# Kernel optimization log

Measured on AMD Instinct MI355X. Metric: run time of the kernel, lower is better.

The kernel has to match this reference:

```python
import jax, jax.numpy as jnp
import numpy as np

N0, N1, N2 = 100000, 20000, 4000   # nodes per hierarchy level
F, H, C = 128, 128, 10             # num_features, hidden_dim, num_classes
E0, E1, E2 = 1600000, 320000, 64000  # intra-level edges (avg degree 16)
EPS = 1e-5                          # BatchNorm eps


def setup_inputs() -> dict:
    key = jax.random.key(0)
    ks = jax.random.split(key, 16)
    s = 0.05
    return {
        "x": jax.random.normal(ks[0], (N0, F), jnp.float32),
        "ei0": jax.random.randint(ks[1], (2, E0), 0, N0),
        "ei1": jax.random.randint(ks[2], (2, E1), 0, N1),
        "ei2": jax.random.randint(ks[3], (2, E2), 0, N2),
        "parent1": jax.random.randint(ks[4], (N0,), 0, N1),
        "parent2": jax.random.randint(ks[5], (N1,), 0, N2),
        "W0": jax.random.normal(ks[6], (F, H), jnp.float32) * s,
        "b0": jnp.zeros((H,), jnp.float32),
        "W1": jax.random.normal(ks[7], (H, H), jnp.float32) * s,
        "b1": jnp.zeros((H,), jnp.float32),
        "W2": jax.random.normal(ks[8], (H, H), jnp.float32) * s,
        "b2": jnp.zeros((H,), jnp.float32),
        "W3": jax.random.normal(ks[9], (2 * H, H), jnp.float32) * s,
        "b3": jnp.zeros((H,), jnp.float32),
        "W4": jax.random.normal(ks[10], (2 * H, C), jnp.float32) * s,
        "b4": jnp.zeros((C,), jnp.float32),
        "pW": jax.random.normal(ks[11], (4, H, H), jnp.float32) * s,
        "pb": jnp.zeros((4, H), jnp.float32),
        "pgamma": jnp.ones((4, H), jnp.float32),
        "pbeta": jnp.zeros((4, H), jnp.float32),
        "pmean": jax.random.normal(ks[12], (4, H), jnp.float32) * 0.1,
        "pvar": jax.random.uniform(ks[13], (4, H), jnp.float32, 0.5, 1.5),
    }


def _gcn(x, ei, W, b):
    # GCNConv: add self loops, symmetric D^-1/2 (A+I) D^-1/2 normalization.
    n = x.shape[0]
    loops = jnp.arange(n)
    row = jnp.concatenate([ei[0], loops])  # source nodes
    col = jnp.concatenate([ei[1], loops])  # target nodes
    deg = jax.ops.segment_sum(jnp.ones(row.shape, x.dtype), col, num_segments=n)
    dis = deg ** -0.5  # deg >= 1 because of self loops
    norm = dis[row] * dis[col]
    xw = x @ W
    out = jax.ops.segment_sum(norm[:, None] * xw[row], col, num_segments=n)
    return out + b


def _pool_nn(y, W, b, g, beta, mean, var):
    # SEPooling nn: Linear -> ReLU -> BatchNorm1d (eval mode, running stats)
    y = jax.nn.relu(y @ W + b)
    return (y - mean) * (g / jnp.sqrt(var + EPS)) + beta


def reference(x, ei0, ei1, ei2, parent1, parent2,
              W0, b0, W1, b1, W2, b2, W3, b3, W4, b4,
              pW, pb, pgamma, pbeta, pmean, pvar):
    relu = jax.nn.relu
    # down path (dropout is identity in eval mode)
    h0 = relu(_gcn(x, ei0, W0, b0))  # [N0,H]; stored skip xs[0]
    p = jax.ops.segment_sum(h0, parent1, num_segments=N1)  # scatter-add children -> parents
    x1 = relu(_pool_nn(p, pW[0], pb[0], pgamma[0], pbeta[0], pmean[0], pvar[0]))
    h1 = relu(_gcn(x1, ei1, W1, b1))  # [N1,H]; stored skip xs[1]
    p = jax.ops.segment_sum(h1, parent2, num_segments=N2)
    x2 = relu(_pool_nn(p, pW[1], pb[1], pgamma[1], pbeta[1], pmean[1], pvar[1]))
    # up path: conv, unpool (gather parent feature per child), concat skip
    h = relu(_gcn(x2, ei2, W2, b2))  # [N2,H]
    xu = relu(_pool_nn(h[parent2], pW[2], pb[2], pgamma[2], pbeta[2], pmean[2], pvar[2]))  # [N1,H]
    xc = jnp.concatenate([xu, h1], axis=1)  # [N1,2H]
    h = relu(_gcn(xc, ei1, W3, b3))  # [N1,H]
    xu = relu(_pool_nn(h[parent1], pW[3], pb[3], pgamma[3], pbeta[3], pmean[3], pvar[3]))  # [N0,H]
    xc = jnp.concatenate([xu, h0], axis=1)  # [N0,2H]
    out = _gcn(xc, ei0, W4, b4)  # [N0,C]
    return jax.nn.log_softmax(out, axis=-1)
```

## Files before the change

kernel.cpp:

```cpp
#include <hip/hip_runtime.h>
#include <math.h>

#define N0 100000
#define N1 20000
#define N2 4000
#define HDIM 128
#define E0C 1600000
#define E1C 320000
#define E2C 64000
#define EPSBN 1e-5f

typedef unsigned int u32;
typedef float f32x4 __attribute__((ext_vector_type(4)));
typedef short bf16x8 __attribute__((ext_vector_type(8)));

union FragU { uint4 u; bf16x8 h; };
__device__ __forceinline__ bf16x8 asbf(uint4 v) { FragU x; x.u = v; return x.h; }

__device__ __forceinline__ float bl(u32 p) { return __uint_as_float(p << 16); }
__device__ __forceinline__ float bh(u32 p) { return __uint_as_float(p & 0xFFFF0000u); }
__device__ __forceinline__ u32 pack2(float a, float b) {
    u32 ua = __float_as_uint(a), ub = __float_as_uint(b);
    ua = (ua + 0x7FFFu + ((ua >> 16) & 1u)) >> 16;
    ub = (ub + 0x7FFFu + ((ub >> 16) & 1u)) >> 16;
    return ua | (ub << 16);
}

#define OFF0 0
#define OFF1 (N0)
#define OFF2 (N0 + N1)
#define OFF3 (N0 + N1 + N2)
#define OFF4 (N0 + N1 + N2 + N1)
#define OFFT (N0 + N1 + N2 + N1 + N2)

#define S0 (E0C)
#define S1 (E0C + E1C)
#define S2 (E0C + E1C + E2C)
#define S3 (E0C + E1C + E2C + N0)
#define S4 (E0C + E1C + E2C + N0 + N1)

#define NBUCK ((OFFT + 1023) / 1024)
#define ITEMS_PER_BLK 4096
#define NBA ((S4 + ITEMS_PER_BLK - 1) / ITEMS_PER_BLK)
#define BH_N (NBUCK * NBA)
#define NBLK2 ((BH_N + 1023) / 1024)


__device__ __forceinline__ void item_full(int g,
    const int* __restrict__ ei0r, const int* __restrict__ ei0c,
    const int* __restrict__ ei1r, const int* __restrict__ ei1c,
    const int* __restrict__ ei2r, const int* __restrict__ ei2c,
    const int* __restrict__ p1, const int* __restrict__ p2,
    int& concat, int& payload)
{
    if (g < S0)      { concat = ei0c[g];             payload = ei0r[g]; }
    else if (g < S1) { int i = g - S0; concat = OFF1 + ei1c[i]; payload = ei1r[i]; }
    else if (g < S2) { int i = g - S1; concat = OFF2 + ei2c[i]; payload = ei2r[i]; }
    else if (g < S3) { int i = g - S2; concat = OFF3 + p1[i];   payload = i; }
    else             { int i = g - S3; concat = OFF4 + p2[i];   payload = i; }
}

__device__ __forceinline__ int item_concat(int g,
    const int* __restrict__ ei0c, const int* __restrict__ ei1c, const int* __restrict__ ei2c,
    const int* __restrict__ p1, const int* __restrict__ p2)
{
    if (g < S0)      return ei0c[g];
    else if (g < S1) return OFF1 + ei1c[g - S0];
    else if (g < S2) return OFF2 + ei2c[g - S1];
    else if (g < S3) return OFF3 + p1[g - S2];
    else             return OFF4 + p2[g - S3];
}

__global__ __launch_bounds__(256) void binhist_kernel(
    const int* __restrict__ ei0c, const int* __restrict__ ei1c, const int* __restrict__ ei2c,
    const int* __restrict__ p1, const int* __restrict__ p2,
    int* __restrict__ blockHist)
{
    __shared__ int hist[NBUCK];
    int tid = threadIdx.x, blk = blockIdx.x;
    for (int i = tid; i < NBUCK; i += 256) hist[i] = 0;
    __syncthreads();
    int base = blk * ITEMS_PER_BLK;
    #pragma unroll
    for (int k = 0; k < 16; k++) {
        int g = base + k * 256 + tid;
        if (g < S4) {
            int c = item_concat(g, ei0c, ei1c, ei2c, p1, p2);
            atomicAdd(&hist[c >> 10], 1);
        }
    }
    __syncthreads();
    for (int b = tid; b < NBUCK; b += 256) blockHist[b * NBA + blk] = hist[b];
}

__global__ __launch_bounds__(256) void scan_k1(const int* __restrict__ c, int* __restrict__ bsum, int n) {
    int t = threadIdx.x;
    int base = blockIdx.x * 1024 + t * 4;
    int s = 0;
    #pragma unroll
    for (int j = 0; j < 4; j++) {
        int idx = base + j;
        if (idx < n) s += c[idx];
    }
    #pragma unroll
    for (int o = 32; o > 0; o >>= 1) s += __shfl_down(s, o, 64);
    __shared__ int ws[4];
    if ((t & 63) == 0) ws[t >> 6] = s;
    __syncthreads();
    if (t == 0) bsum[blockIdx.x] = ws[0] + ws[1] + ws[2] + ws[3];
}

__global__ __launch_bounds__(256) void scan_k2(int* __restrict__ bsum, int* __restrict__ totalOut, int nb) {
    int t = threadIdx.x;
    int v = (t < nb) ? bsum[t] : 0;
    __shared__ int ts[256];
    ts[t] = v;
    __syncthreads();
    for (int o = 1; o < 256; o <<= 1) {
        int u = (t >= o) ? ts[t - o] : 0;
        __syncthreads();
        ts[t] += u;
        __syncthreads();
    }
    if (t < nb) bsum[t] = ts[t] - v;
    if (t == nb - 1) *totalOut = ts[t];
}

__global__ __launch_bounds__(256) void scan_k3(const int* __restrict__ c, const int* __restrict__ bsum,
                                               const int* __restrict__ total,
                                               int* __restrict__ S, int n) {
    int t = threadIdx.x;
    int base = blockIdx.x * 1024 + t * 4;
    int v[4];
    #pragma unroll
    for (int j = 0; j < 4; j++) v[j] = (base + j < n) ? c[base + j] : 0;
    int tsum = v[0] + v[1] + v[2] + v[3];
    __shared__ int ts[256];
    ts[t] = tsum;
    __syncthreads();
    for (int o = 1; o < 256; o <<= 1) {
        int u = (t >= o) ? ts[t - o] : 0;
        __syncthreads();
        ts[t] += u;
        __syncthreads();
    }
    int run = bsum[blockIdx.x] + ts[t] - tsum;
    #pragma unroll
    for (int j = 0; j < 4; j++) {
        if (base + j < n) { S[base + j] = run; run += v[j]; }
    }
    if (blockIdx.x == 0 && t == 0) S[n] = *total;
}

__global__ __launch_bounds__(256) void binfill_kernel(
    const int* __restrict__ ei0r, const int* __restrict__ ei0c,
    const int* __restrict__ ei1r, const int* __restrict__ ei1c,
    const int* __restrict__ ei2r, const int* __restrict__ ei2c,
    const int* __restrict__ p1, const int* __restrict__ p2,
    const int* __restrict__ OfsAbs, u32* __restrict__ binPair)
{
    __shared__ int cur[NBUCK];
    int tid = threadIdx.x, blk = blockIdx.x;
    for (int i = tid; i < NBUCK; i += 256) cur[i] = OfsAbs[i * NBA + blk];
    __syncthreads();
    int base = blk * ITEMS_PER_BLK;
    #pragma unroll
    for (int k = 0; k < 16; k++) {
        int g = base + k * 256 + tid;
        if (g < S4) {
            int c, p;
            item_full(g, ei0r, ei0c, ei1r, ei1c, ei2r, ei2c, p1, p2, c, p);
            int pos = atomicAdd(&cur[c >> 10], 1);
            binPair[pos] = ((u32)(c & 1023) << 17) | (u32)p;
        }
    }
}

__global__ __launch_bounds__(256) void bucket_build_kernel(
    const u32* __restrict__ binPair, const int* __restrict__ OfsAbs,
    int* __restrict__ rpAll, int* __restrict__ srcU,
    float* __restrict__ dis0, float* __restrict__ dis1, float* __restrict__ dis2)
{
    __shared__ int cnt_l[1024];
    __shared__ int rp_l[1024];
    __shared__ int ts[256];
    int b = blockIdx.x, tid = threadIdx.x;
    int start = OfsAbs[b * NBA];
    int end = (b + 1 < NBUCK) ? OfsAbs[(b + 1) * NBA] : S4;
    int d0 = b << 10;
    int nd = OFFT - d0; if (nd > 1024) nd = 1024;

    for (int i = tid; i < 1024; i += 256) cnt_l[i] = 0;
    __syncthreads();
    for (int i = start + tid; i < end; i += 256) {
        u32 e = binPair[i];
        atomicAdd(&cnt_l[e >> 17], 1);
    }
    __syncthreads();
    int bi = tid * 4;
    int v0 = cnt_l[bi], v1 = cnt_l[bi + 1], v2 = cnt_l[bi + 2], v3 = cnt_l[bi + 3];
    int tsum = v0 + v1 + v2 + v3;
    ts[tid] = tsum;
    __syncthreads();
    for (int o = 1; o < 256; o <<= 1) {
        int u = (tid >= o) ? ts[tid - o] : 0;
        __syncthreads();
        ts[tid] += u;
        __syncthreads();
    }
    int run = ts[tid] - tsum;
    rp_l[bi] = run;
    rp_l[bi + 1] = run + v0;
    rp_l[bi + 2] = run + v0 + v1;
    rp_l[bi + 3] = run + v0 + v1 + v2;
    __syncthreads();
    for (int j = tid; j < nd; j += 256) {
        int g = d0 + j;
        rpAll[g] = start + rp_l[j];
        int c = cnt_l[j];
        float dv = rsqrtf((float)(c + 1));
        if (g < OFF1) dis0[g] = dv;
        else if (g < OFF2) dis1[g - OFF1] = dv;
        else if (g < OFF3) dis2[g - OFF2] = dv;
    }
    if (b == NBUCK - 1 && tid == 0) rpAll[OFFT] = S4;
    __syncthreads();
    for (int i = start + tid; i < end; i += 256) {
        u32 e = binPair[i];
        int pos = start + atomicAdd(&rp_l[e >> 17], 1);
        srcU[pos] = (int)(e & 0x1FFFFu);
    }
}

__global__ void bn_pre_kernel(const float* __restrict__ g, const float* __restrict__ beta,
                              const float* __restrict__ mean, const float* __restrict__ var,
                              float* __restrict__ scale, float* __restrict__ shift) {
    int i = blockIdx.x * blockDim.x + threadIdx.x;
    if (i < 4 * HDIM) {
        float s = g[i] * rsqrtf(var[i] + EPSBN);
        scale[i] = s;
        shift[i] = beta[i] - mean[i] * s;
    }
}


#define G128_LOAD(sym, off) u32 sym = y[(long long)srcl[e + off] * 64 + lane]

__global__ __launch_bounds__(256) void gather128_kernel(
    const int* __restrict__ rp, const int* __restrict__ srcl,
    const u32* __restrict__ y, const float* __restrict__ dis,
    const float* __restrict__ bias, u32* __restrict__ h, int n)
{
    int wid = (int)((blockIdx.x * 256 + threadIdx.x) >> 6);
    int lane = threadIdx.x & 63;
    if (wid >= n) return;
    u32 self = y[(long long)wid * 64 + lane];
    float ax = bl(self), ay = bh(self);
    int e = rp[wid], e1 = rp[wid + 1];
    for (; e + 15 < e1; e += 16) {
        G128_LOAD(p0, 0); G128_LOAD(p1, 1); G128_LOAD(p2, 2); G128_LOAD(p3, 3);
        G128_LOAD(p4, 4); G128_LOAD(p5, 5); G128_LOAD(p6, 6); G128_LOAD(p7, 7);
        G128_LOAD(p8, 8); G128_LOAD(p9, 9); G128_LOAD(pa, 10); G128_LOAD(pb, 11);
        G128_LOAD(pc, 12); G128_LOAD(pd, 13); G128_LOAD(pe, 14); G128_LOAD(pf, 15);
        ax += (((bl(p0) + bl(p1)) + (bl(p2) + bl(p3))) + ((bl(p4) + bl(p5)) + (bl(p6) + bl(p7))))
            + (((bl(p8) + bl(p9)) + (bl(pa) + bl(pb))) + ((bl(pc) + bl(pd)) + (bl(pe) + bl(pf))));
        ay += (((bh(p0) + bh(p1)) + (bh(p2) + bh(p3))) + ((bh(p4) + bh(p5)) + (bh(p6) + bh(p7))))
            + (((bh(p8) + bh(p9)) + (bh(pa) + bh(pb))) + ((bh(pc) + bh(pd)) + (bh(pe) + bh(pf))));
    }
    if (e + 7 < e1) {
        G128_LOAD(p0, 0); G128_LOAD(p1, 1); G128_LOAD(p2, 2); G128_LOAD(p3, 3);
        G128_LOAD(p4, 4); G128_LOAD(p5, 5); G128_LOAD(p6, 6); G128_LOAD(p7, 7);
        ax += ((bl(p0) + bl(p1)) + (bl(p2) + bl(p3))) + ((bl(p4) + bl(p5)) + (bl(p6) + bl(p7)));
        ay += ((bh(p0) + bh(p1)) + (bh(p2) + bh(p3))) + ((bh(p4) + bh(p5)) + (bh(p6) + bh(p7)));
        e += 8;
    }
    if (e + 3 < e1) {
        G128_LOAD(p0, 0); G128_LOAD(p1, 1); G128_LOAD(p2, 2); G128_LOAD(p3, 3);
        ax += (bl(p0) + bl(p1)) + (bl(p2) + bl(p3));
        ay += (bh(p0) + bh(p1)) + (bh(p2) + bh(p3));
        e += 4;
    }
    if (e + 1 < e1) {
        G128_LOAD(p0, 0); G128_LOAD(p1, 1);
        ax += bl(p0) + bl(p1);
        ay += bh(p0) + bh(p1);
        e += 2;
    }
    if (e < e1) {
        G128_LOAD(p0, 0);
        ax += bl(p0); ay += bh(p0);
    }
    float d = dis[wid];
    float2 b = ((const float2*)bias)[lane];
    float r0 = fmaxf(fmaf(d, ax, b.x), 0.f);
    float r1 = fmaxf(fmaf(d, ay, b.y), 0.f);
    h[(long long)wid * 64 + lane] = pack2(r0, r1);
}

#define GP_LOAD(sym, off) u32 sym = h[(long long)childl[e + off] * 64 + lane]

__global__ __launch_bounds__(256) void gatherP_kernel(
    const int* __restrict__ pp, const int* __restrict__ childl,
    const u32* __restrict__ h, u32* __restrict__ p, int n)
{
    int wid = (int)((blockIdx.x * 256 + threadIdx.x) >> 6);
    int lane = threadIdx.x & 63;
    if (wid >= n) return;
    float ax = 0.f, ay = 0.f;
    int e = pp[wid], e1 = pp[wid + 1];
    for (; e + 7 < e1; e += 8) {
        GP_LOAD(p0, 0); GP_LOAD(p1, 1); GP_LOAD(p2, 2); GP_LOAD(p3, 3);
        GP_LOAD(p4, 4); GP_LOAD(p5, 5); GP_LOAD(p6, 6); GP_LOAD(p7, 7);
        ax += ((bl(p0) + bl(p1)) + (bl(p2) + bl(p3))) + ((bl(p4) + bl(p5)) + (bl(p6) + bl(p7)));
        ay += ((bh(p0) + bh(p1)) + (bh(p2) + bh(p3))) + ((bh(p4) + bh(p5)) + (bh(p6) + bh(p7)));
    }
    if (e + 3 < e1) {
        GP_LOAD(p0, 0); GP_LOAD(p1, 1); GP_LOAD(p2, 2); GP_LOAD(p3, 3);
        ax += (bl(p0) + bl(p1)) + (bl(p2) + bl(p3));
        ay += (bh(p0) + bh(p1)) + (bh(p2) + bh(p3));
        e += 4;
    }
    if (e + 1 < e1) {
        GP_LOAD(p0, 0); GP_LOAD(p1, 1);
        ax += bl(p0) + bl(p1);
        ay += bh(p0) + bh(p1);
        e += 2;
    }
    if (e < e1) {
        GP_LOAD(p0, 0);
        ax += bl(p0); ay += bh(p0);
    }
    p[(long long)wid * 64 + lane] = pack2(ax, ay);
}

__global__ __launch_bounds__(256) void gather10_lsm_kernel(
    const int* __restrict__ rp, const int* __restrict__ srcl,
    const u32* __restrict__ y4, const float* __restrict__ dis,
    const float* __restrict__ bias, float* __restrict__ out, int n)
{
    int c = blockIdx.x * blockDim.x + threadIdx.x;
    if (c >= n) return;
    float acc[10];
    {
        long long base = (long long)c * 8;
        uint4 q = *(const uint4*)(y4 + base);
        u32 q4 = y4[base + 4];
        acc[0] = bl(q.x); acc[1] = bh(q.x);
        acc[2] = bl(q.y); acc[3] = bh(q.y);
        acc[4] = bl(q.z); acc[5] = bh(q.z);
        acc[6] = bl(q.w); acc[7] = bh(q.w);
        acc[8] = bl(q4);  acc[9] = bh(q4);
    }
    int e = rp[c], e1 = rp[c + 1];
    for (; e + 3 < e1; e += 4) {
        long long bA = (long long)srcl[e] * 8;
        long long bB = (long long)srcl[e + 1] * 8;
        long long bC = (long long)srcl[e + 2] * 8;
        long long bD = (long long)srcl[e + 3] * 8;
        uint4 qa = *(const uint4*)(y4 + bA); u32 qa4 = y4[bA + 4];
        uint4 qb = *(const uint4*)(y4 + bB); u32 qb4 = y4[bB + 4];
        uint4 qc = *(const uint4*)(y4 + bC); u32 qc4 = y4[bC + 4];
        uint4 qd = *(const uint4*)(y4 + bD); u32 qd4 = y4[bD + 4];
        acc[0] += (bl(qa.x) + bl(qb.x)) + (bl(qc.x) + bl(qd.x));
        acc[1] += (bh(qa.x) + bh(qb.x)) + (bh(qc.x) + bh(qd.x));
        acc[2] += (bl(qa.y) + bl(qb.y)) + (bl(qc.y) + bl(qd.y));
        acc[3] += (bh(qa.y) + bh(qb.y)) + (bh(qc.y) + bh(qd.y));
        acc[4] += (bl(qa.z) + bl(qb.z)) + (bl(qc.z) + bl(qd.z));
        acc[5] += (bh(qa.z) + bh(qb.z)) + (bh(qc.z) + bh(qd.z));
        acc[6] += (bl(qa.w) + bl(qb.w)) + (bl(qc.w) + bl(qd.w));
        acc[7] += (bh(qa.w) + bh(qb.w)) + (bh(qc.w) + bh(qd.w));
        acc[8] += (bl(qa4) + bl(qb4)) + (bl(qc4) + bl(qd4));
        acc[9] += (bh(qa4) + bh(qb4)) + (bh(qc4) + bh(qd4));
    }
    for (; e < e1; e++) {
        long long bA = (long long)srcl[e] * 8;
        uint4 qa = *(const uint4*)(y4 + bA);
        u32 qa4 = y4[bA + 4];
        acc[0] += bl(qa.x); acc[1] += bh(qa.x);
        acc[2] += bl(qa.y); acc[3] += bh(qa.y);
        acc[4] += bl(qa.z); acc[5] += bh(qa.z);
        acc[6] += bl(qa.w); acc[7] += bh(qa.w);
        acc[8] += bl(qa4);  acc[9] += bh(qa4);
    }
    float d = dis[c];
    float m = -1e30f;
    #pragma unroll
    for (int k = 0; k < 10; k++) {
        acc[k] = fmaf(d, acc[k], bias[k]);
        m = fmaxf(m, acc[k]);
    }
    float s = 0.f;
    #pragma unroll
    for (int k = 0; k < 10; k++) s += expf(acc[k] - m);
    float ls = logf(s);
    #pragma unroll
    for (int k = 0; k < 10; k++) out[(long long)c * 10 + k] = acc[k] - m - ls;
}

__global__ __launch_bounds__(256) void mm128_kernel(
    const void* __restrict__ Av, const float* __restrict__ W,
    u32* __restrict__ out, int M,
    const float* __restrict__ dis,
    const u32* __restrict__ gsrc, const int* __restrict__ gidx,
    const float* __restrict__ bias,
    const float* __restrict__ bnscale, const float* __restrict__ bnshift,
    int pool, int afp32)
{
    __shared__ u32 WL[8192];
    int tid = threadIdx.x;

    #pragma unroll
    for (int it = 0; it < 32; it++) {
        int flat = it * 256 + tid;
        int i = flat & 3;
        int ln = (flat >> 2) & 63;
        int s = (flat >> 8) & 3;
        int t = flat >> 10;
        int mm = ln & 15, qq = ln >> 4;
        int k0 = s * 32 + qq * 8 + 2 * i;
        int col = t * 16 + mm;
        WL[flat] = pack2(W[k0 * 128 + col], W[(k0 + 1) * 128 + col]);
    }
    __syncthreads();

    int lane = tid & 63;
    int w = tid >> 6;
    int m = lane & 15, q = lane >> 4;
    int row = blockIdx.x * 64 + w * 16 + m;
    bool live = (row < M);

    uint4 xb[4];
    if (live) {
        if (afp32) {
            const float* Af = (const float*)Av;
            #pragma unroll
            for (int s = 0; s < 4; s++) {
                const float4* p = (const float4*)(Af + (long long)row * 128 + s * 32 + q * 8);
                float4 f0 = p[0], f1 = p[1];
                xb[s].x = pack2(f0.x, f0.y);
                xb[s].y = pack2(f0.z, f0.w);
                xb[s].z = pack2(f1.x, f1.y);
                xb[s].w = pack2(f1.z, f1.w);
            }
        } else {
            const u32* Ab = (const u32*)Av;
            #pragma unroll
            for (int s = 0; s < 4; s++)
                xb[s] = *(const uint4*)(Ab + (long long)row * 64 + s * 16 + q * 4);
        }
    } else {
        xb[0] = xb[1] = xb[2] = xb[3] = make_uint4(0u, 0u, 0u, 0u);
    }

    float d = 1.0f;
    if (dis && live) d = dis[row];
    long long gbase = (gsrc && live) ? (long long)gidx[row] * 64 : 0;

    #pragma unroll
    for (int t = 0; t < 8; t++) {
        f32x4 acc = {0.f, 0.f, 0.f, 0.f};
        #pragma unroll
        for (int s = 0; s < 4; s++) {
            uint4 wa = *(const uint4*)&WL[((t * 4 + s) * 64 + lane) * 4];
            acc = __builtin_amdgcn_mfma_f32_16x16x32_bf16(asbf(wa), asbf(xb[s]), acc, 0, 0, 0);
        }
        if (live) {
            float v0 = acc[0], v1 = acc[1], v2 = acc[2], v3 = acc[3];
            int cbase = t * 16 + q * 4;
            if (gsrc) {
                uint2 g = *(const uint2*)(gsrc + gbase + (cbase >> 1));
                v0 += bl(g.x); v1 += bh(g.x);
                v2 += bl(g.y); v3 += bh(g.y);
            }
            if (pool) {
                float4 bb = *(const float4*)(bias + cbase);
                float4 sc = *(const float4*)(bnscale + cbase);
                float4 sh = *(const float4*)(bnshift + cbase);
                v0 = fmaxf(fmaxf(v0 + bb.x, 0.f) * sc.x + sh.x, 0.f);
                v1 = fmaxf(fmaxf(v1 + bb.y, 0.f) * sc.y + sh.y, 0.f);
                v2 = fmaxf(fmaxf(v2 + bb.z, 0.f) * sc.z + sh.z, 0.f);
                v3 = fmaxf(fmaxf(v3 + bb.w, 0.f) * sc.w + sh.w, 0.f);
            }
            v0 *= d; v1 *= d; v2 *= d; v3 *= d;
            uint2 st;
            st.x = pack2(v0, v1);
            st.y = pack2(v2, v3);
            *(uint2*)(out + (long long)row * 64 + (cbase >> 1)) = st;
        }
    }
}

__global__ __launch_bounds__(256) void mm10_kernel(
    const u32* __restrict__ A, const float* __restrict__ W,
    float* __restrict__ out, int M)
{
    __shared__ float Ws[128 * 10];
    for (int i = threadIdx.x; i < 1280; i += 256) Ws[i] = W[i];
    __syncthreads();
    int row = blockIdx.x * blockDim.x + threadIdx.x;
    if (row >= M) return;
    const uint4* a = (const uint4*)(A + (long long)row * 64);
    float acc[10] = {0, 0, 0, 0, 0, 0, 0, 0, 0, 0};
    #pragma unroll 4
    for (int i = 0; i < 16; i++) {
        uint4 av = a[i];
        int k = i * 8;
        float f[8] = { bl(av.x), bh(av.x), bl(av.y), bh(av.y),
                       bl(av.z), bh(av.z), bl(av.w), bh(av.w) };
        #pragma unroll
        for (int j = 0; j < 8; j++) {
            #pragma unroll
            for (int cc = 0; cc < 10; cc++)
                acc[cc] += f[j] * Ws[(k + j) * 10 + cc];
        }
    }
    #pragma unroll
    for (int cc = 0; cc < 10; cc++) out[(long long)row * 10 + cc] = acc[cc];
}

__global__ __launch_bounds__(256) void mm10p_kernel(
    const u32* __restrict__ A, const float* __restrict__ W,
    u32* __restrict__ outp, int M,
    const float* __restrict__ dis,
    const float* __restrict__ gsrc, const int* __restrict__ gidx)
{
    __shared__ float Ws[128 * 10];
    for (int i = threadIdx.x; i < 1280; i += 256) Ws[i] = W[i];
    __syncthreads();
    int row = blockIdx.x * blockDim.x + threadIdx.x;
    if (row >= M) return;
    const uint4* a = (const uint4*)(A + (long long)row * 64);
    float acc[10] = {0, 0, 0, 0, 0, 0, 0, 0, 0, 0};
    #pragma unroll 4
    for (int i = 0; i < 16; i++) {
        uint4 av = a[i];
        int k = i * 8;
        float f[8] = { bl(av.x), bh(av.x), bl(av.y), bh(av.y),
                       bl(av.z), bh(av.z), bl(av.w), bh(av.w) };
        #pragma unroll
        for (int j = 0; j < 8; j++) {
            #pragma unroll
            for (int cc = 0; cc < 10; cc++)
                acc[cc] += f[j] * Ws[(k + j) * 10 + cc];
        }
    }
    float d = dis[row];
    const float* g = gsrc + (long long)gidx[row] * 10;
    long long base = (long long)row * 8;
    #pragma unroll
    for (int j = 0; j < 5; j++) {
        float v0 = (acc[2 * j] + g[2 * j]) * d;
        float v1 = (acc[2 * j + 1] + g[2 * j + 1]) * d;
        outp[base + j] = pack2(v0, v1);
    }
}


extern "C" void kernel_launch(void* const* d_in, const int* in_sizes, int n_in,
                              void* d_out, int out_size, void* d_ws, size_t ws_size,
                              hipStream_t stream) {
    const float* x       = (const float*)d_in[0];
    const int*   ei0     = (const int*)d_in[1];
    const int*   ei1     = (const int*)d_in[2];
    const int*   ei2     = (const int*)d_in[3];
    const int*   parent1 = (const int*)d_in[4];
    const int*   parent2 = (const int*)d_in[5];
    const float* W0 = (const float*)d_in[6];
    const float* b0 = (const float*)d_in[7];
    const float* W1 = (const float*)d_in[8];
    const float* b1 = (const float*)d_in[9];
    const float* W2 = (const float*)d_in[10];
    const float* b2 = (const float*)d_in[11];
    const float* W3 = (const float*)d_in[12];
    const float* b3 = (const float*)d_in[13];
    const float* W4 = (const float*)d_in[14];
    const float* b4 = (const float*)d_in[15];
    const float* pW = (const float*)d_in[16];
    const float* pb = (const float*)d_in[17];
    const float* pg = (const float*)d_in[18];
    const float* pbeta = (const float*)d_in[19];
    const float* pmean = (const float*)d_in[20];
    const float* pvar  = (const float*)d_in[21];
    float* out = (float*)d_out;

    char* ws = (char*)d_ws;
    size_t off = 0;
    auto alloc = [&](size_t nbytes) -> char* {
        char* p = ws + off;
        off += ((nbytes + 255) / 256) * 256;
        return p;
    };
    float* dis0 = (float*)alloc(N0 * 4);
    float* dis1 = (float*)alloc(N1 * 4);
    float* dis2 = (float*)alloc(N2 * 4);
    float* bnscale = (float*)alloc(4 * HDIM * 4);
    float* bnshift = (float*)alloc(4 * HDIM * 4);
    float* W1b = (float*)alloc((size_t)N1 * 10 * 4);
    u32* Y   = (u32*)alloc((size_t)N0 * 64 * 4);
    u32* H0  = (u32*)alloc((size_t)N0 * 64 * 4);
    u32* H1  = (u32*)alloc((size_t)N1 * 64 * 4);
    u32* P   = (u32*)alloc((size_t)N1 * 64 * 4);
    u32* X1  = (u32*)alloc((size_t)N1 * 64 * 4);
    u32* HU1 = (u32*)alloc((size_t)N1 * 64 * 4);
    u32* U1  = (u32*)alloc((size_t)N1 * 64 * 4);
    u32* X2  = (u32*)alloc((size_t)N2 * 64 * 4);
    u32* H2  = (u32*)alloc((size_t)N2 * 64 * 4);
    u32* U2  = (u32*)alloc((size_t)N2 * 64 * 4);
    u32* V2  = (u32*)alloc((size_t)N2 * 64 * 4);
    u32* Y4p = (u32*)alloc((size_t)N0 * 8 * 4);
    int* rpAll = (int*)alloc((size_t)(OFFT + 1) * 4);
    int* srcU  = (int*)alloc((size_t)S4 * 4);
    int* blockHist = (int*)alloc((size_t)BH_N * 4);
    int* OfsAbs    = (int*)alloc((size_t)(BH_N + 1) * 4);
    u32* binPair   = (u32*)alloc((size_t)S4 * 4);
    int* bsum   = (int*)alloc(NBLK2 * 4);
    int* totalb = (int*)alloc(4);

    const int B = 256;
    auto G = [](long long t) { return (unsigned)((t + 255) / 256); };
    auto G64 = [](long long m) { return (unsigned)((m + 63) / 64); };

    binhist_kernel<<<NBA, B, 0, stream>>>(
        ei0 + E0C, ei1 + E1C, ei2 + E2C, parent1, parent2, blockHist);
    scan_k1<<<NBLK2, B, 0, stream>>>(blockHist, bsum, BH_N);
    scan_k2<<<1, B, 0, stream>>>(bsum, totalb, NBLK2);
    scan_k3<<<NBLK2, B, 0, stream>>>(blockHist, bsum, totalb, OfsAbs, BH_N);
    binfill_kernel<<<NBA, B, 0, stream>>>(
        ei0, ei0 + E0C, ei1, ei1 + E1C, ei2, ei2 + E2C, parent1, parent2, OfsAbs, binPair);
    bucket_build_kernel<<<NBUCK, B, 0, stream>>>(
        binPair, OfsAbs, rpAll, srcU, dis0, dis1, dis2);
    bn_pre_kernel<<<2, B, 0, stream>>>(pg, pbeta, pmean, pvar, bnscale, bnshift);

    mm128_kernel<<<G64(N0), B, 0, stream>>>(
        x, W0, Y, N0, dis0, nullptr, nullptr, nullptr, nullptr, nullptr, 0, 1);
    gather128_kernel<<<G((long long)N0 * 64), B, 0, stream>>>(rpAll + OFF0, srcU, Y, dis0, b0, H0, N0);

    gatherP_kernel<<<G((long long)N1 * 64), B, 0, stream>>>(rpAll + OFF3, srcU, H0, P, N1);
    mm128_kernel<<<G64(N1), B, 0, stream>>>(
        P, pW, X1, N1, nullptr, nullptr, nullptr, pb, bnscale, bnshift, 1, 0);

    mm128_kernel<<<G64(N1), B, 0, stream>>>(
        X1, W1, Y, N1, dis1, nullptr, nullptr, nullptr, nullptr, nullptr, 0, 0);
    gather128_kernel<<<G((long long)N1 * 64), B, 0, stream>>>(rpAll + OFF1, srcU, Y, dis1, b1, H1, N1);

    gatherP_kernel<<<G((long long)N2 * 64), B, 0, stream>>>(rpAll + OFF4, srcU, H1, P, N2);
    mm128_kernel<<<G64(N2), B, 0, stream>>>(
        P, pW + 128 * 128, X2, N2, nullptr, nullptr, nullptr, pb + 128, bnscale + 128, bnshift + 128, 1, 0);

    mm128_kernel<<<G64(N2), B, 0, stream>>>(
        X2, W2, Y, N2, dis2, nullptr, nullptr, nullptr, nullptr, nullptr, 0, 0);
    gather128_kernel<<<G((long long)N2 * 64), B, 0, stream>>>(rpAll + OFF2, srcU, Y, dis2, b2, H2, N2);

    mm128_kernel<<<G64(N2), B, 0, stream>>>(
        H2, pW + 2 * 128 * 128, U2, N2, nullptr, nullptr, nullptr, pb + 256, bnscale + 256, bnshift + 256, 1, 0);
    mm128_kernel<<<G64(N2), B, 0, stream>>>(
        U2, W3, V2, N2, nullptr, nullptr, nullptr, nullptr, nullptr, nullptr, 0, 0);

    mm128_kernel<<<G64(N1), B, 0, stream>>>(
        H1, W3 + 128 * 128, Y, N1, dis1, V2, parent2, nullptr, nullptr, nullptr, 0, 0);
    gather128_kernel<<<G((long long)N1 * 64), B, 0, stream>>>(rpAll + OFF1, srcU, Y, dis1, b3, HU1, N1);

    mm128_kernel<<<G64(N1), B, 0, stream>>>(
        HU1, pW + 3 * 128 * 128, U1, N1, nullptr, nullptr, nullptr, pb + 384, bnscale + 384, bnshift + 384, 1, 0);
    mm10_kernel<<<G(N1), B, 0, stream>>>(U1, W4, W1b, N1);

    mm10p_kernel<<<G(N0), B, 0, stream>>>(H0, W4 + 128 * 10, Y4p, N0, dis0, W1b, parent1);
    gather10_lsm_kernel<<<G(N0), B, 0, stream>>>(rpAll + OFF0, srcU, Y4p, dis0, b4, out, N0);
}
```

Measured before the change: 447.4 us.

## Fuse pooling gather into matmul, widen bucket build, shrink CSR item blocks

Removes the separate gatherP kernel and its P buffer by summing child rows directly inside mm128's A-operand load, selected by a new apool flag. Halves ITEMS_PER_BLK for the histogram and fill kernels, which doubles their block count. Rewrites bucket_build to run 1024 threads with one node per thread and a 1024-wide scan, and drops the 16-edge unroll in gather128. The fused pool load runs a serial per-row loop with many registers and fewer threads per row, which may reduce memory parallelism, and the longer scan adds barriers.

```diff
diff --git a/kernel.cpp b/kernel.cpp
--- a/kernel.cpp
+++ b/kernel.cpp
@@ -40,7 +40,7 @@
 #define S4 (E0C + E1C + E2C + N0 + N1)
 
 #define NBUCK ((OFFT + 1023) / 1024)
-#define ITEMS_PER_BLK 4096
+#define ITEMS_PER_BLK 2048
 #define NBA ((S4 + ITEMS_PER_BLK - 1) / ITEMS_PER_BLK)
 #define BH_N (NBUCK * NBA)
 #define NBLK2 ((BH_N + 1023) / 1024)
@@ -82,7 +82,7 @@
     __syncthreads();
     int base = blk * ITEMS_PER_BLK;
     #pragma unroll
-    for (int k = 0; k < 16; k++) {
+    for (int k = 0; k < ITEMS_PER_BLK / 256; k++) {
         int g = base + k * 256 + tid;
         if (g < S4) {
             int c = item_concat(g, ei0c, ei1c, ei2c, p1, p2);
@@ -165,7 +165,7 @@
     __syncthreads();
     int base = blk * ITEMS_PER_BLK;
     #pragma unroll
-    for (int k = 0; k < 16; k++) {
+    for (int k = 0; k < ITEMS_PER_BLK / 256; k++) {
         int g = base + k * 256 + tid;
         if (g < S4) {
             int c, p;
@@ -176,56 +176,49 @@
     }
 }
 
-__global__ __launch_bounds__(256) void bucket_build_kernel(
+__global__ __launch_bounds__(1024) void bucket_build_kernel(
     const u32* __restrict__ binPair, const int* __restrict__ OfsAbs,
     int* __restrict__ rpAll, int* __restrict__ srcU,
     float* __restrict__ dis0, float* __restrict__ dis1, float* __restrict__ dis2)
 {
     __shared__ int cnt_l[1024];
     __shared__ int rp_l[1024];
-    __shared__ int ts[256];
+    __shared__ int ts2[1024];
     int b = blockIdx.x, tid = threadIdx.x;
     int start = OfsAbs[b * NBA];
     int end = (b + 1 < NBUCK) ? OfsAbs[(b + 1) * NBA] : S4;
     int d0 = b << 10;
     int nd = OFFT - d0; if (nd > 1024) nd = 1024;
 
-    for (int i = tid; i < 1024; i += 256) cnt_l[i] = 0;
-    __syncthreads();
-    for (int i = start + tid; i < end; i += 256) {
+    cnt_l[tid] = 0;
+    __syncthreads();
+    for (int i = start + tid; i < end; i += 1024) {
         u32 e = binPair[i];
         atomicAdd(&cnt_l[e >> 17], 1);
     }
     __syncthreads();
-    int bi = tid * 4;
-    int v0 = cnt_l[bi], v1 = cnt_l[bi + 1], v2 = cnt_l[bi + 2], v3 = cnt_l[bi + 3];
-    int tsum = v0 + v1 + v2 + v3;
-    ts[tid] = tsum;
-    __syncthreads();
-    for (int o = 1; o < 256; o <<= 1) {
-        int u = (tid >= o) ? ts[tid - o] : 0;
+    int v = cnt_l[tid];
+    ts2[tid] = v;
+    __syncthreads();
+    for (int o = 1; o < 1024; o <<= 1) {
+        int u = (tid >= o) ? ts2[tid - o] : 0;
         __syncthreads();
-        ts[tid] += u;
+        ts2[tid] += u;
         __syncthreads();
     }
-    int run = ts[tid] - tsum;
-    rp_l[bi] = run;
-    rp_l[bi + 1] = run + v0;
-    rp_l[bi + 2] = run + v0 + v1;
-    rp_l[bi + 3] = run + v0 + v1 + v2;
-    __syncthreads();
-    for (int j = tid; j < nd; j += 256) {
-        int g = d0 + j;
-        rpAll[g] = start + rp_l[j];
-        int c = cnt_l[j];
-        float dv = rsqrtf((float)(c + 1));
+    rp_l[tid] = ts2[tid] - v;
+    __syncthreads();
+    if (tid < nd) {
+        int g = d0 + tid;
+        rpAll[g] = start + rp_l[tid];
+        float dv = rsqrtf((float)(v + 1));
         if (g < OFF1) dis0[g] = dv;
         else if (g < OFF2) dis1[g - OFF1] = dv;
         else if (g < OFF3) dis2[g - OFF2] = dv;
     }
     if (b == NBUCK - 1 && tid == 0) rpAll[OFFT] = S4;
     __syncthreads();
-    for (int i = start + tid; i < end; i += 256) {
+    for (int i = start + tid; i < end; i += 1024) {
         u32 e = binPair[i];
         int pos = start + atomicAdd(&rp_l[e >> 17], 1);
         srcU[pos] = (int)(e & 0x1FFFFu);
@@ -257,22 +250,11 @@
     u32 self = y[(long long)wid * 64 + lane];
     float ax = bl(self), ay = bh(self);
     int e = rp[wid], e1 = rp[wid + 1];
-    for (; e + 15 < e1; e += 16) {
-        G128_LOAD(p0, 0); G128_LOAD(p1, 1); G128_LOAD(p2, 2); G128_LOAD(p3, 3);
-        G128_LOAD(p4, 4); G128_LOAD(p5, 5); G128_LOAD(p6, 6); G128_LOAD(p7, 7);
-        G128_LOAD(p8, 8); G128_LOAD(p9, 9); G128_LOAD(pa, 10); G128_LOAD(pb, 11);
-        G128_LOAD(pc, 12); G128_LOAD(pd, 13); G128_LOAD(pe, 14); G128_LOAD(pf, 15);
-        ax += (((bl(p0) + bl(p1)) + (bl(p2) + bl(p3))) + ((bl(p4) + bl(p5)) + (bl(p6) + bl(p7))))
-            + (((bl(p8) + bl(p9)) + (bl(pa) + bl(pb))) + ((bl(pc) + bl(pd)) + (bl(pe) + bl(pf))));
-        ay += (((bh(p0) + bh(p1)) + (bh(p2) + bh(p3))) + ((bh(p4) + bh(p5)) + (bh(p6) + bh(p7))))
-            + (((bh(p8) + bh(p9)) + (bh(pa) + bh(pb))) + ((bh(pc) + bh(pd)) + (bh(pe) + bh(pf))));
-    }
-    if (e + 7 < e1) {
+    for (; e + 7 < e1; e += 8) {
         G128_LOAD(p0, 0); G128_LOAD(p1, 1); G128_LOAD(p2, 2); G128_LOAD(p3, 3);
         G128_LOAD(p4, 4); G128_LOAD(p5, 5); G128_LOAD(p6, 6); G128_LOAD(p7, 7);
         ax += ((bl(p0) + bl(p1)) + (bl(p2) + bl(p3))) + ((bl(p4) + bl(p5)) + (bl(p6) + bl(p7)));
         ay += ((bh(p0) + bh(p1)) + (bh(p2) + bh(p3))) + ((bh(p4) + bh(p5)) + (bh(p6) + bh(p7)));
-        e += 8;
     }
     if (e + 3 < e1) {
         G128_LOAD(p0, 0); G128_LOAD(p1, 1); G128_LOAD(p2, 2); G128_LOAD(p3, 3);
@@ -295,42 +277,6 @@
     float r0 = fmaxf(fmaf(d, ax, b.x), 0.f);
     float r1 = fmaxf(fmaf(d, ay, b.y), 0.f);
     h[(long long)wid * 64 + lane] = pack2(r0, r1);
-}
-
-#define GP_LOAD(sym, off) u32 sym = h[(long long)childl[e + off] * 64 + lane]
-
-__global__ __launch_bounds__(256) void gatherP_kernel(
-    const int* __restrict__ pp, const int* __restrict__ childl,
-    const u32* __restrict__ h, u32* __restrict__ p, int n)
-{
-    int wid = (int)((blockIdx.x * 256 + threadIdx.x) >> 6);
-    int lane = threadIdx.x & 63;
-    if (wid >= n) return;
-    float ax = 0.f, ay = 0.f;
-    int e = pp[wid], e1 = pp[wid + 1];
-    for (; e + 7 < e1; e += 8) {
-        GP_LOAD(p0, 0); GP_LOAD(p1, 1); GP_LOAD(p2, 2); GP_LOAD(p3, 3);
-        GP_LOAD(p4, 4); GP_LOAD(p5, 5); GP_LOAD(p6, 6); GP_LOAD(p7, 7);
-        ax += ((bl(p0) + bl(p1)) + (bl(p2) + bl(p3))) + ((bl(p4) + bl(p5)) + (bl(p6) + bl(p7)));
-        ay += ((bh(p0) + bh(p1)) + (bh(p2) + bh(p3))) + ((bh(p4) + bh(p5)) + (bh(p6) + bh(p7)));
-    }
-    if (e + 3 < e1) {
-        GP_LOAD(p0, 0); GP_LOAD(p1, 1); GP_LOAD(p2, 2); GP_LOAD(p3, 3);
-        ax += (bl(p0) + bl(p1)) + (bl(p2) + bl(p3));
-        ay += (bh(p0) + bh(p1)) + (bh(p2) + bh(p3));
-        e += 4;
-    }
-    if (e + 1 < e1) {
-        GP_LOAD(p0, 0); GP_LOAD(p1, 1);
-        ax += bl(p0) + bl(p1);
-        ay += bh(p0) + bh(p1);
-        e += 2;
-    }
-    if (e < e1) {
-        GP_LOAD(p0, 0);
-        ax += bl(p0); ay += bh(p0);
-    }
-    p[(long long)wid * 64 + lane] = pack2(ax, ay);
 }
 
 __global__ __launch_bounds__(256) void gather10_lsm_kernel(
@@ -404,7 +350,8 @@
     const u32* __restrict__ gsrc, const int* __restrict__ gidx,
     const float* __restrict__ bias,
     const float* __restrict__ bnscale, const float* __restrict__ bnshift,
-    int pool, int afp32)
+    int pool, int afp32,
+    const int* __restrict__ pp, const int* __restrict__ childl, int apool)
 {
     __shared__ u32 WL[8192];
     int tid = threadIdx.x;
@@ -431,7 +378,31 @@
 
     uint4 xb[4];
     if (live) {
-        if (afp32) {
+        if (apool) {
+            float fa[32];
+            #pragma unroll
+            for (int i = 0; i < 32; i++) fa[i] = 0.f;
+            const u32* Hb = (const u32*)Av;
+            int e = pp[row], eE = pp[row + 1];
+            for (; e < eE; e++) {
+                long long cb = (long long)childl[e] * 64;
+                #pragma unroll
+                for (int s = 0; s < 4; s++) {
+                    uint4 vv = *(const uint4*)(Hb + cb + s * 16 + q * 4);
+                    fa[s * 8 + 0] += bl(vv.x); fa[s * 8 + 1] += bh(vv.x);
+                    fa[s * 8 + 2] += bl(vv.y); fa[s * 8 + 3] += bh(vv.y);
+                    fa[s * 8 + 4] += bl(vv.z); fa[s * 8 + 5] += bh(vv.z);
+                    fa[s * 8 + 6] += bl(vv.w); fa[s * 8 + 7] += bh(vv.w);
+                }
+            }
+            #pragma unroll
+            for (int s = 0; s < 4; s++) {
+                xb[s].x = pack2(fa[s * 8 + 0], fa[s * 8 + 1]);
+                xb[s].y = pack2(fa[s * 8 + 2], fa[s * 8 + 3]);
+                xb[s].z = pack2(fa[s * 8 + 4], fa[s * 8 + 5]);
+                xb[s].w = pack2(fa[s * 8 + 6], fa[s * 8 + 7]);
+            }
+        } else if (afp32) {
             const float* Af = (const float*)Av;
             #pragma unroll
             for (int s = 0; s < 4; s++) {
@@ -599,7 +570,6 @@
     u32* Y   = (u32*)alloc((size_t)N0 * 64 * 4);
     u32* H0  = (u32*)alloc((size_t)N0 * 64 * 4);
     u32* H1  = (u32*)alloc((size_t)N1 * 64 * 4);
-    u32* P   = (u32*)alloc((size_t)N1 * 64 * 4);
     u32* X1  = (u32*)alloc((size_t)N1 * 64 * 4);
     u32* HU1 = (u32*)alloc((size_t)N1 * 64 * 4);
     u32* U1  = (u32*)alloc((size_t)N1 * 64 * 4);
@@ -627,41 +597,48 @@
     scan_k3<<<NBLK2, B, 0, stream>>>(blockHist, bsum, totalb, OfsAbs, BH_N);
     binfill_kernel<<<NBA, B, 0, stream>>>(
         ei0, ei0 + E0C, ei1, ei1 + E1C, ei2, ei2 + E2C, parent1, parent2, OfsAbs, binPair);
-    bucket_build_kernel<<<NBUCK, B, 0, stream>>>(
+    bucket_build_kernel<<<NBUCK, 1024, 0, stream>>>(
         binPair, OfsAbs, rpAll, srcU, dis0, dis1, dis2);
     bn_pre_kernel<<<2, B, 0, stream>>>(pg, pbeta, pmean, pvar, bnscale, bnshift);
 
     mm128_kernel<<<G64(N0), B, 0, stream>>>(
-        x, W0, Y, N0, dis0, nullptr, nullptr, nullptr, nullptr, nullptr, 0, 1);
+        x, W0, Y, N0, dis0, nullptr, nullptr, nullptr, nullptr, nullptr, 0, 1,
+        nullptr, nullptr, 0);
     gather128_kernel<<<G((long long)N0 * 64), B, 0, stream>>>(rpAll + OFF0, srcU, Y, dis0, b0, H0, N0);
 
-    gatherP_kernel<<<G((long long)N1 * 64), B, 0, stream>>>(rpAll + OFF3, srcU, H0, P, N1);
     mm128_kernel<<<G64(N1), B, 0, stream>>>(
-        P, pW, X1, N1, nullptr, nullptr, nullptr, pb, bnscale, bnshift, 1, 0);
+        H0, pW, X1, N1, nullptr, nullptr, nullptr, pb, bnscale, bnshift, 1, 0,
+        rpAll + OFF3, srcU, 1);
 
     mm128_kernel<<<G64(N1), B, 0, stream>>>(
-        X1, W1, Y, N1, dis1, nullptr, nullptr, nullptr, nullptr, nullptr, 0, 0);
+        X1, W1, Y, N1, dis1, nullptr, nullptr, nullptr, nullptr, nullptr, 0, 0,
+        nullptr, nullptr, 0);
     gather128_kernel<<<G((long long)N1 * 64), B, 0, stream>>>(rpAll + OFF1, srcU, Y, dis1, b1, H1, N1);
 
-    gatherP_kernel<<<G((long long)N2 * 64), B, 0, stream>>>(rpAll + OFF4, srcU, H1, P, N2);
     mm128_kernel<<<G64(N2), B, 0, stream>>>(
-        P, pW + 128 * 128, X2, N2, nullptr, nullptr, nullptr, pb + 128, bnscale + 128, bnshift + 128, 1, 0);
+        H1, pW + 128 * 128, X2, N2, nullptr, nullptr, nullptr, pb + 128, bnscale + 128, bnshift + 128, 1, 0,
+        rpAll + OFF4, srcU, 1);
 
     mm128_kernel<<<G64(N2), B, 0, stream>>>(
-        X2, W2, Y, N2, dis2, nullptr, nullptr, nullptr, nullptr, nullptr, 0, 0);
+        X2, W2, Y, N2, dis2, nullptr, nullptr, nullptr, nullptr, nullptr, 0, 0,
+        nullptr, nullptr, 0);
     gather128_kernel<<<G((long long)N2 * 64), B, 0, stream>>>(rpAll + OFF2, srcU, Y, dis2, b2, H2, N2);
 
     mm128_kernel<<<G64(N2), B, 0, stream>>>(
-        H2, pW + 2 * 128 * 128, U2, N2, nullptr, nullptr, nullptr, pb + 256, bnscale + 256, bnshift + 256, 1, 0);
+        H2, pW + 2 * 128 * 128, U2, N2, nullptr, nullptr, nullptr, pb + 256, bnscale + 256, bnshift + 256, 1, 0,
+        nullptr, nullptr, 0);
     mm128_kernel<<<G64(N2), B, 0, stream>>>(
-        U2, W3, V2, N2, nullptr, nullptr, nullptr, nullptr, nullptr, nullptr, 0, 0);
+        U2, W3, V2, N2, nullptr, nullptr, nullptr, nullptr, nullptr, nullptr, 0, 0,
+        nullptr, nullptr, 0);
 
     mm128_kernel<<<G64(N1), B, 0, stream>>>(
-        H1, W3 + 128 * 128, Y, N1, dis1, V2, parent2, nullptr, nullptr, nullptr, 0, 0);
+        H1, W3 + 128 * 128, Y, N1, dis1, V2, parent2, nullptr, nullptr, nullptr, 0, 0,
+        nullptr, nullptr, 0);
     gather128_kernel<<<G((long long)N1 * 64), B, 0, stream>>>(rpAll + OFF1, srcU, Y, dis1, b3, HU1, N1);
 
     mm128_kernel<<<G64(N1), B, 0, stream>>>(
-        HU1, pW + 3 * 128 * 128, U1, N1, nullptr, nullptr, nullptr, pb + 384, bnscale + 384, bnshift + 384, 1, 0);
+        HU1, pW + 3 * 128 * 128, U1, N1, nullptr, nullptr, nullptr, pb + 384, bnscale + 384, bnshift + 384, 1, 0,
+        nullptr, nullptr, 0);
     mm10_kernel<<<G(N1), B, 0, stream>>>(U1, W4, W1b, N1);
 
     mm10p_kernel<<<G(N0), B, 0, stream>>>(H0, W4 + 128 * 10, Y4p, N0, dis0, W1b, parent1);
```

Measured after the change: 431.8 us. -3.5%, faster.
